# Kernel tuning notes

Measured on AMD Instinct MI355X. Metric: run time of the kernel, lower is better.

Reference implementation:

```python
import jax, jax.numpy as jnp
import numpy as np

D_MODEL = 1024
N_HEADS = 16
HEAD_DIM = D_MODEL // N_HEADS
B, S = 2, 2048


def setup_inputs() -> dict:
    key = jax.random.key(0)
    ks = jax.random.split(key, 10)
    q = jax.random.normal(ks[0], (B, S, D_MODEL), dtype=jnp.float32)
    k = jax.random.normal(ks[1], (B, S, D_MODEL), dtype=jnp.float32)
    v = jax.random.normal(ks[2], (B, S, D_MODEL), dtype=jnp.float32)
    # causal mask: 1 where attention is forbidden (upper triangle), 0 elsewhere
    mask = jnp.triu(jnp.ones((S, S), dtype=jnp.float32), k=1)[None, None, :, :]
    scale = 0.02
    Wk = jax.random.normal(ks[3], (D_MODEL, D_MODEL), dtype=jnp.float32) * scale
    bk = jnp.zeros((D_MODEL,), dtype=jnp.float32)
    Wv = jax.random.normal(ks[4], (D_MODEL, D_MODEL), dtype=jnp.float32) * scale
    bv = jnp.zeros((D_MODEL,), dtype=jnp.float32)
    Wo = jax.random.normal(ks[5], (D_MODEL, D_MODEL), dtype=jnp.float32) * scale
    bo = jnp.zeros((D_MODEL,), dtype=jnp.float32)
    return {"query": q, "key": k, "value": v, "mask": mask,
            "Wk": Wk, "bk": bk, "Wv": Wv, "bv": bv, "Wo": Wo, "bo": bo}


def reference(query, key, value, mask, Wk, bk, Wv, bv, Wo, bo):
    b, s, d = query.shape
    h, dh = N_HEADS, HEAD_DIM

    def split(x):  # [b, s, d] -> [b, h, s, dh]
        return x.reshape(b, -1, h, dh).transpose(0, 2, 1, 3)

    # NOTE: faithful to source bug — query is projected with weights_key.
    q = split(query @ Wk.T + bk)
    k = split(key @ Wk.T + bk)
    v = split(value @ Wv.T + bv)

    inv_sqrt_dh = jnp.float32(1.0 / np.sqrt(dh))
    scores = jnp.einsum('bhqd,bhkd->bhqk', q, k) * inv_sqrt_dh
    scores = scores + mask * jnp.float32(-1e9)
    w = jax.nn.softmax(scores, axis=-1)           # [b, h, s, s]
    ctx = jnp.einsum('bhqk,bhkd->bhqd', w, v)     # [b, h, s, dh]
    concat = ctx.transpose(0, 2, 1, 3).reshape(b, -1, d)
    out = concat @ Wo.T + bo
    return (out, w)
```

## Files before the change

### kernel.cpp

```cpp
#include <hip/hip_runtime.h>
#include <stdint.h>

#define BB 2
#define SS 2048
#define DD 1024
#define HH 16
#define DH 64
#define MM 4096

typedef unsigned short u16;
typedef __attribute__((ext_vector_type(8))) __bf16 bf16x8;
typedef __attribute__((ext_vector_type(4))) float f32x4;

__device__ __forceinline__ u16 f2bf(float f) {
    union { float f; unsigned int u; } x; x.f = f;
    unsigned int u = x.u;
    return (u16)((u + 0x7fffu + ((u >> 16) & 1u)) >> 16);
}

__global__ __launch_bounds__(256) void cvt_kernel(const float* __restrict__ src,
                                                  u16* __restrict__ dst, int n4) {
    int i = blockIdx.x * 256 + threadIdx.x;
    if (i < n4) {
        float4 v = ((const float4*)src)[i];
        ushort4 o;
        o.x = f2bf(v.x); o.y = f2bf(v.y); o.z = f2bf(v.z); o.w = f2bf(v.w);
        ((ushort4*)dst)[i] = o;
    }
}

template <int OUT_MODE>
__device__ __forceinline__ void gemm_core(u16* As, u16* Bs,
                                          const u16* __restrict__ A,
                                          const u16* __restrict__ W,
                                          const float* __restrict__ bias,
                                          void* __restrict__ Cout,
                                          int bx, int by) {
    const int tid = threadIdx.x;
    const int lane = tid & 63, wid = tid >> 6;
    const int wy = wid >> 1, wx = wid & 1;
    const int quad = lane >> 4, cl = lane & 15;
    const int m0 = by * 128, n0 = bx * 128;

    f32x4 acc[4][4];
#pragma unroll
    for (int i = 0; i < 4; ++i)
#pragma unroll
        for (int j = 0; j < 4; ++j) acc[i][j] = (f32x4){0.f, 0.f, 0.f, 0.f};

    for (int kt = 0; kt < 1024; kt += 32) {
        __syncthreads();
#pragma unroll
        for (int j = 0; j < 2; ++j) {
            int ch = j * 256 + tid;
            int row = ch >> 2, ko = (ch & 3) * 8;
            uint4 va = *(const uint4*)(A + (size_t)(m0 + row) * 1024 + kt + ko);
            uint4 vb = *(const uint4*)(W + (size_t)(n0 + row) * 1024 + kt + ko);
            *(uint4*)(As + row * 40 + ko) = va;
            *(uint4*)(Bs + row * 40 + ko) = vb;
        }
        __syncthreads();
        bf16x8 af[4], bfr[4];
#pragma unroll
        for (int t = 0; t < 4; ++t) {
            af[t]  = *(const bf16x8*)(As + (wy * 64 + t * 16 + cl) * 40 + quad * 8);
            bfr[t] = *(const bf16x8*)(Bs + (wx * 64 + t * 16 + cl) * 40 + quad * 8);
        }
#pragma unroll
        for (int mt = 0; mt < 4; ++mt)
#pragma unroll
            for (int nt = 0; nt < 4; ++nt)
                acc[mt][nt] = __builtin_amdgcn_mfma_f32_16x16x32_bf16(
                    af[mt], bfr[nt], acc[mt][nt], 0, 0, 0);
    }

#pragma unroll
    for (int mt = 0; mt < 4; ++mt) {
#pragma unroll
        for (int nt = 0; nt < 4; ++nt) {
            int n = n0 + wx * 64 + nt * 16 + cl;
            float bv = bias[n];
#pragma unroll
            for (int r = 0; r < 4; ++r) {
                int m = m0 + wy * 64 + mt * 16 + quad * 4 + r;
                float v = acc[mt][nt][r] + bv;
                if (OUT_MODE == 0) {
                    int b = m >> 11, s = m & 2047, h = n >> 6, d = n & 63;
                    ((u16*)Cout)[((size_t)(b * 16 + h) * 2048 + s) * 64 + d] = f2bf(v);
                } else if (OUT_MODE == 1) {
                    int b = m >> 11, s = m & 2047, h = n >> 6, d = n & 63;
                    ((u16*)Cout)[((size_t)(b * 16 + h) * 64 + d) * 2048 + s] = f2bf(v);
                } else {
                    ((float*)Cout)[(size_t)m * 1024 + n] = v;
                }
            }
        }
    }
}

__global__ __launch_bounds__(256, 2) void proj_kernel(
    const u16* __restrict__ Xq, const u16* __restrict__ Xk, const u16* __restrict__ Xv,
    const u16* __restrict__ Wkb, const u16* __restrict__ Wvb,
    const float* __restrict__ bk, const float* __restrict__ bv,
    u16* __restrict__ Qh, u16* __restrict__ Kh, u16* __restrict__ Vt) {
    __shared__ u16 As[128 * 40];
    __shared__ u16 Bs[128 * 40];
    int z = blockIdx.z;
    const u16* A = (z == 0) ? Xq : (z == 1) ? Xk : Xv;
    const u16* W = (z == 2) ? Wvb : Wkb;
    const float* bias = (z == 2) ? bv : bk;
    if (z == 2)
        gemm_core<1>(As, Bs, A, W, bias, Vt, blockIdx.x, blockIdx.y);
    else
        gemm_core<0>(As, Bs, A, W, bias, (z == 0) ? (void*)Qh : (void*)Kh,
                     blockIdx.x, blockIdx.y);
}

__global__ __launch_bounds__(256, 2) void outproj_kernel(
    const u16* __restrict__ Ctx, const u16* __restrict__ Wob,
    const float* __restrict__ bo, float* __restrict__ out) {
    __shared__ u16 As[128 * 40];
    __shared__ u16 Bs[128 * 40];
    gemm_core<2>(As, Bs, Ctx, Wob, bo, out, blockIdx.x, blockIdx.y);
}

__global__ __launch_bounds__(256, 2) void attn_kernel(
    const u16* __restrict__ Qh, const u16* __restrict__ Kh, const u16* __restrict__ Vt,
    float* __restrict__ Wout, u16* __restrict__ Ctx) {
    __shared__ u16 Ks[64 * 72];
    __shared__ u16 Vs[64 * 72];
    __shared__ u16 Ps[128 * 72];

    const int tid = threadIdx.x;
    const int lane = tid & 63, wid = tid >> 6;
    const int quad = lane >> 4, cl = lane & 15;
    const int qb = blockIdx.x, bh = blockIdx.y;
    const int q0 = qb * 128;
    const int b = bh >> 4, h = bh & 15;

    const u16* Qp = Qh + (size_t)bh * 2048 * 64;
    const u16* Kp = Kh + (size_t)bh * 2048 * 64;
    const u16* Vp = Vt + (size_t)bh * 64 * 2048;
    float* Wp = Wout + (size_t)bh * 2048 * 2048;

    bf16x8 qf[2][2];
#pragma unroll
    for (int mt = 0; mt < 2; ++mt)
#pragma unroll
        for (int ks = 0; ks < 2; ++ks) {
            int row = q0 + wid * 32 + mt * 16 + cl;
            qf[mt][ks] = *(const bf16x8*)(Qp + (size_t)row * 64 + ks * 32 + quad * 8);
        }

    float mrun[8], lrun[8];
#pragma unroll
    for (int i = 0; i < 8; ++i) { mrun[i] = -1e30f; lrun[i] = 0.f; }

    const int nkt = 2 * qb + 2;

    for (int kt = 0; kt < nkt; ++kt) {
        __syncthreads();
#pragma unroll
        for (int j = 0; j < 2; ++j) {
            int ch = j * 256 + tid;
            int row = ch >> 3, ko = (ch & 7) * 8;
            *(uint4*)(Ks + row * 72 + ko) =
                *(const uint4*)(Kp + (size_t)(kt * 64 + row) * 64 + ko);
        }
        __syncthreads();

        f32x4 sc[2][4];
#pragma unroll
        for (int nt = 0; nt < 4; ++nt) {
            bf16x8 kf0 = *(const bf16x8*)(Ks + (nt * 16 + cl) * 72 + quad * 8);
            bf16x8 kf1 = *(const bf16x8*)(Ks + (nt * 16 + cl) * 72 + 32 + quad * 8);
#pragma unroll
            for (int mt = 0; mt < 2; ++mt) {
                f32x4 a = (f32x4){0.f, 0.f, 0.f, 0.f};
                a = __builtin_amdgcn_mfma_f32_16x16x32_bf16(qf[mt][0], kf0, a, 0, 0, 0);
                a = __builtin_amdgcn_mfma_f32_16x16x32_bf16(qf[mt][1], kf1, a, 0, 0, 0);
                sc[mt][nt] = a;
            }
        }
#pragma unroll
        for (int mt = 0; mt < 2; ++mt)
#pragma unroll
            for (int r = 0; r < 4; ++r) {
                int li = mt * 4 + r;
                int grow = q0 + wid * 32 + mt * 16 + quad * 4 + r;
                float tmax = -1e30f;
#pragma unroll
                for (int nt = 0; nt < 4; ++nt) {
                    int gcol = kt * 64 + nt * 16 + cl;
                    float s = sc[mt][nt][r] * 0.125f;
                    s = (gcol <= grow) ? s : -1e30f;
                    sc[mt][nt][r] = s;
                    tmax = fmaxf(tmax, s);
                }
#pragma unroll
                for (int off = 1; off < 16; off <<= 1)
                    tmax = fmaxf(tmax, __shfl_xor(tmax, off));
                float mnew = fmaxf(mrun[li], tmax);
                float sum = 0.f;
#pragma unroll
                for (int nt = 0; nt < 4; ++nt)
                    sum += __expf(sc[mt][nt][r] - mnew);
#pragma unroll
                for (int off = 1; off < 16; off <<= 1)
                    sum += __shfl_xor(sum, off);
                lrun[li] = lrun[li] * __expf(mrun[li] - mnew) + sum;
                mrun[li] = mnew;
            }
    }

    float rli[8];
#pragma unroll
    for (int i = 0; i < 8; ++i) rli[i] = 1.0f / lrun[i];

    f32x4 ctx[2][4];
#pragma unroll
    for (int mt = 0; mt < 2; ++mt)
#pragma unroll
        for (int d = 0; d < 4; ++d) ctx[mt][d] = (f32x4){0.f, 0.f, 0.f, 0.f};

    for (int kt = 0; kt < nkt; ++kt) {
        __syncthreads();
#pragma unroll
        for (int j = 0; j < 2; ++j) {
            int ch = j * 256 + tid;
            int row = ch >> 3, ko = (ch & 7) * 8;
            *(uint4*)(Ks + row * 72 + ko) =
                *(const uint4*)(Kp + (size_t)(kt * 64 + row) * 64 + ko);
            *(uint4*)(Vs + row * 72 + ko) =
                *(const uint4*)(Vp + (size_t)row * 2048 + kt * 64 + ko);
        }
        __syncthreads();

        f32x4 sc[2][4];
#pragma unroll
        for (int nt = 0; nt < 4; ++nt) {
            bf16x8 kf0 = *(const bf16x8*)(Ks + (nt * 16 + cl) * 72 + quad * 8);
            bf16x8 kf1 = *(const bf16x8*)(Ks + (nt * 16 + cl) * 72 + 32 + quad * 8);
#pragma unroll
            for (int mt = 0; mt < 2; ++mt) {
                f32x4 a = (f32x4){0.f, 0.f, 0.f, 0.f};
                a = __builtin_amdgcn_mfma_f32_16x16x32_bf16(qf[mt][0], kf0, a, 0, 0, 0);
                a = __builtin_amdgcn_mfma_f32_16x16x32_bf16(qf[mt][1], kf1, a, 0, 0, 0);
                sc[mt][nt] = a;
            }
        }
#pragma unroll
        for (int mt = 0; mt < 2; ++mt)
#pragma unroll
            for (int r = 0; r < 4; ++r) {
                int li = mt * 4 + r;
                int lrow = wid * 32 + mt * 16 + quad * 4 + r;
                int grow = q0 + lrow;
                float mm = mrun[li], rl = rli[li];
#pragma unroll
                for (int nt = 0; nt < 4; ++nt) {
                    int gcol = kt * 64 + nt * 16 + cl;
                    float s = sc[mt][nt][r] * 0.125f;
                    s = (gcol <= grow) ? s : -1e30f;
                    float p = __expf(s - mm);
                    Wp[(size_t)grow * 2048 + gcol] = p * rl;
                    Ps[lrow * 72 + nt * 16 + cl] = f2bf(p);
                }
            }
        __syncthreads();

#pragma unroll
        for (int ks = 0; ks < 2; ++ks) {
            bf16x8 pf[2];
#pragma unroll
            for (int mt = 0; mt < 2; ++mt)
                pf[mt] = *(const bf16x8*)(Ps + (wid * 32 + mt * 16 + cl) * 72 + ks * 32 + quad * 8);
#pragma unroll
            for (int d = 0; d < 4; ++d) {
                bf16x8 vf = *(const bf16x8*)(Vs + (d * 16 + cl) * 72 + ks * 32 + quad * 8);
#pragma unroll
                for (int mt = 0; mt < 2; ++mt)
                    ctx[mt][d] = __builtin_amdgcn_mfma_f32_16x16x32_bf16(
                        pf[mt], vf, ctx[mt][d], 0, 0, 0);
            }
        }
    }

    for (int zt = qb + 1; zt < 16; ++zt) {
        float4 z = {0.f, 0.f, 0.f, 0.f};
#pragma unroll
        for (int j = 0; j < 16; ++j) {
            int idx = j * 256 + tid;
            int row = idx >> 5, col4 = idx & 31;
            *(float4*)(Wp + (size_t)(q0 + row) * 2048 + zt * 128 + col4 * 4) = z;
        }
    }

#pragma unroll
    for (int mt = 0; mt < 2; ++mt)
#pragma unroll
        for (int d = 0; d < 4; ++d)
#pragma unroll
            for (int r = 0; r < 4; ++r) {
                int li = mt * 4 + r;
                int grow = q0 + wid * 32 + mt * 16 + quad * 4 + r;
                int col = d * 16 + cl;
                float v = ctx[mt][d][r] * rli[li];
                Ctx[((size_t)(b * 2048 + grow)) * 1024 + h * 64 + col] = f2bf(v);
            }
}

extern "C" void kernel_launch(void* const* d_in, const int* in_sizes, int n_in,
                              void* d_out, int out_size, void* d_ws, size_t ws_size,
                              hipStream_t stream) {
    const float* qin = (const float*)d_in[0];
    const float* kin = (const float*)d_in[1];
    const float* vin = (const float*)d_in[2];
    const float* Wk = (const float*)d_in[4];
    const float* bk = (const float*)d_in[5];
    const float* Wv = (const float*)d_in[6];
    const float* bv = (const float*)d_in[7];
    const float* Wo = (const float*)d_in[8];
    const float* bo = (const float*)d_in[9];

    float* outp = (float*)d_out;
    float* wout = outp + (size_t)MM * DD;

    u16* Xq  = (u16*)d_ws;
    u16* Xk  = Xq  + (size_t)MM * DD;
    u16* Xv  = Xk  + (size_t)MM * DD;
    u16* Wkb = Xv  + (size_t)MM * DD;
    u16* Wvb = Wkb + (size_t)DD * DD;
    u16* Wob = Wvb + (size_t)DD * DD;
    u16* Qh  = Wob + (size_t)DD * DD;
    u16* Kh  = Qh  + (size_t)MM * DD;
    u16* Vt  = Kh  + (size_t)MM * DD;
    u16* Ctx = Vt  + (size_t)MM * DD;

    dim3 blk(256, 1, 1);
    cvt_kernel<<<dim3(MM * DD / 4 / 256, 1, 1), blk, 0, stream>>>(qin, Xq, MM * DD / 4);
    cvt_kernel<<<dim3(MM * DD / 4 / 256, 1, 1), blk, 0, stream>>>(kin, Xk, MM * DD / 4);
    cvt_kernel<<<dim3(MM * DD / 4 / 256, 1, 1), blk, 0, stream>>>(vin, Xv, MM * DD / 4);
    cvt_kernel<<<dim3(DD * DD / 4 / 256, 1, 1), blk, 0, stream>>>(Wk, Wkb, DD * DD / 4);
    cvt_kernel<<<dim3(DD * DD / 4 / 256, 1, 1), blk, 0, stream>>>(Wv, Wvb, DD * DD / 4);
    cvt_kernel<<<dim3(DD * DD / 4 / 256, 1, 1), blk, 0, stream>>>(Wo, Wob, DD * DD / 4);

    proj_kernel<<<dim3(8, 32, 3), blk, 0, stream>>>(Xq, Xk, Xv, Wkb, Wvb, bk, bv, Qh, Kh, Vt);
    attn_kernel<<<dim3(16, 32, 1), blk, 0, stream>>>(Qh, Kh, Vt, wout, Ctx);
    outproj_kernel<<<dim3(8, 32, 1), blk, 0, stream>>>(Ctx, Wob, bo, outp);
}
```

Before: 786.5 us.

## Use direct global-to-LDS loads, causal load balancing, nontemporal stores, and skip unneeded masking

The GEMM tile loads now use global_load_lds to copy straight into unpadded LDS instead of staging through registers. This drops the register round trip but may add LDS bank conflicts because the padding is gone. The attention kernel reverses the q-block order for odd batches to balance causal work across blocks, and applies the causal mask only on diagonal tiles. The large probability-matrix writes and the zero fills use nontemporal stores. A block-wide barrier before the P@V step is replaced with a wave-local lgkmcnt wait, which holds only because each wave reads back its own rows of Ps.

```diff
diff --git a/kernel.cpp b/kernel.cpp
--- a/kernel.cpp
+++ b/kernel.cpp
@@ -16,6 +16,12 @@
     union { float f; unsigned int u; } x; x.f = f;
     unsigned int u = x.u;
     return (u16)((u + 0x7fffu + ((u >> 16) & 1u)) >> 16);
+}
+
+__device__ __forceinline__ void gl_lds16(const u16* g, u16* l) {
+    __builtin_amdgcn_global_load_lds(
+        (const __attribute__((address_space(1))) unsigned int*)g,
+        (__attribute__((address_space(3))) unsigned int*)l, 16, 0, 0);
 }
 
 __global__ __launch_bounds__(256) void cvt_kernel(const float* __restrict__ src,
@@ -48,23 +54,25 @@
 #pragma unroll
         for (int j = 0; j < 4; ++j) acc[i][j] = (f32x4){0.f, 0.f, 0.f, 0.f};
 
+    const int ch0 = tid;
+    const int row0 = ch0 >> 2, ko0 = (ch0 & 3) * 8;
+    const int ch1 = 256 + tid;
+    const int row1 = ch1 >> 2, ko1 = (ch1 & 3) * 8;
+    const int lb0 = (wid * 64) * 8;
+    const int lb1 = (256 + wid * 64) * 8;
+
     for (int kt = 0; kt < 1024; kt += 32) {
         __syncthreads();
-#pragma unroll
-        for (int j = 0; j < 2; ++j) {
-            int ch = j * 256 + tid;
-            int row = ch >> 2, ko = (ch & 3) * 8;
-            uint4 va = *(const uint4*)(A + (size_t)(m0 + row) * 1024 + kt + ko);
-            uint4 vb = *(const uint4*)(W + (size_t)(n0 + row) * 1024 + kt + ko);
-            *(uint4*)(As + row * 40 + ko) = va;
-            *(uint4*)(Bs + row * 40 + ko) = vb;
-        }
+        gl_lds16(A + (size_t)(m0 + row0) * 1024 + kt + ko0, As + lb0);
+        gl_lds16(W + (size_t)(n0 + row0) * 1024 + kt + ko0, Bs + lb0);
+        gl_lds16(A + (size_t)(m0 + row1) * 1024 + kt + ko1, As + lb1);
+        gl_lds16(W + (size_t)(n0 + row1) * 1024 + kt + ko1, Bs + lb1);
         __syncthreads();
         bf16x8 af[4], bfr[4];
 #pragma unroll
         for (int t = 0; t < 4; ++t) {
-            af[t]  = *(const bf16x8*)(As + (wy * 64 + t * 16 + cl) * 40 + quad * 8);
-            bfr[t] = *(const bf16x8*)(Bs + (wx * 64 + t * 16 + cl) * 40 + quad * 8);
+            af[t]  = *(const bf16x8*)(As + (wy * 64 + t * 16 + cl) * 32 + quad * 8);
+            bfr[t] = *(const bf16x8*)(Bs + (wx * 64 + t * 16 + cl) * 32 + quad * 8);
         }
 #pragma unroll
         for (int mt = 0; mt < 4; ++mt)
@@ -103,8 +111,8 @@
     const u16* __restrict__ Wkb, const u16* __restrict__ Wvb,
     const float* __restrict__ bk, const float* __restrict__ bv,
     u16* __restrict__ Qh, u16* __restrict__ Kh, u16* __restrict__ Vt) {
-    __shared__ u16 As[128 * 40];
-    __shared__ u16 Bs[128 * 40];
+    __shared__ u16 As[128 * 32];
+    __shared__ u16 Bs[128 * 32];
     int z = blockIdx.z;
     const u16* A = (z == 0) ? Xq : (z == 1) ? Xk : Xv;
     const u16* W = (z == 2) ? Wvb : Wkb;
@@ -119,8 +127,8 @@
 __global__ __launch_bounds__(256, 2) void outproj_kernel(
     const u16* __restrict__ Ctx, const u16* __restrict__ Wob,
     const float* __restrict__ bo, float* __restrict__ out) {
-    __shared__ u16 As[128 * 40];
-    __shared__ u16 Bs[128 * 40];
+    __shared__ u16 As[128 * 32];
+    __shared__ u16 Bs[128 * 32];
     gemm_core<2>(As, Bs, Ctx, Wob, bo, out, blockIdx.x, blockIdx.y);
 }
 
@@ -134,7 +142,8 @@
     const int tid = threadIdx.x;
     const int lane = tid & 63, wid = tid >> 6;
     const int quad = lane >> 4, cl = lane & 15;
-    const int qb = blockIdx.x, bh = blockIdx.y;
+    const int bh = blockIdx.y;
+    const int qb = ((bh >> 4) & 1) ? (15 - (int)blockIdx.x) : (int)blockIdx.x;
     const int q0 = qb * 128;
     const int b = bh >> 4, h = bh & 15;
 
@@ -169,6 +178,7 @@
         }
         __syncthreads();
 
+        const bool tile_masked = (kt >= 2 * qb);
         f32x4 sc[2][4];
 #pragma unroll
         for (int nt = 0; nt < 4; ++nt) {
@@ -193,7 +203,7 @@
                 for (int nt = 0; nt < 4; ++nt) {
                     int gcol = kt * 64 + nt * 16 + cl;
                     float s = sc[mt][nt][r] * 0.125f;
-                    s = (gcol <= grow) ? s : -1e30f;
+                    if (tile_masked) s = (gcol <= grow) ? s : -1e30f;
                     sc[mt][nt][r] = s;
                     tmax = fmaxf(tmax, s);
                 }
@@ -236,6 +246,7 @@
         }
         __syncthreads();
 
+        const bool tile_masked = (kt >= 2 * qb);
         f32x4 sc[2][4];
 #pragma unroll
         for (int nt = 0; nt < 4; ++nt) {
@@ -261,13 +272,13 @@
                 for (int nt = 0; nt < 4; ++nt) {
                     int gcol = kt * 64 + nt * 16 + cl;
                     float s = sc[mt][nt][r] * 0.125f;
-                    s = (gcol <= grow) ? s : -1e30f;
+                    if (tile_masked) s = (gcol <= grow) ? s : -1e30f;
                     float p = __expf(s - mm);
-                    Wp[(size_t)grow * 2048 + gcol] = p * rl;
+                    __builtin_nontemporal_store(p * rl, Wp + (size_t)grow * 2048 + gcol);
                     Ps[lrow * 72 + nt * 16 + cl] = f2bf(p);
                 }
             }
-        __syncthreads();
+        asm volatile("s_waitcnt lgkmcnt(0)" ::: "memory");
 
 #pragma unroll
         for (int ks = 0; ks < 2; ++ks) {
@@ -287,12 +298,13 @@
     }
 
     for (int zt = qb + 1; zt < 16; ++zt) {
-        float4 z = {0.f, 0.f, 0.f, 0.f};
+        f32x4 z = (f32x4){0.f, 0.f, 0.f, 0.f};
 #pragma unroll
         for (int j = 0; j < 16; ++j) {
             int idx = j * 256 + tid;
             int row = idx >> 5, col4 = idx & 31;
-            *(float4*)(Wp + (size_t)(q0 + row) * 2048 + zt * 128 + col4 * 4) = z;
+            __builtin_nontemporal_store(
+                z, (f32x4*)(Wp + (size_t)(q0 + row) * 2048 + zt * 128 + col4 * 4));
         }
     }
 
```

Result: faster. 762.3 us (-3.1%).
